# Performance work log

Measured on AMD Instinct MI355X. Metric: run time of the kernel, lower is better.

## Reference

```python
import jax, jax.numpy as jnp
import numpy as np

# --- fan-beam (flat detector) FBP geometry constants, matching init geo dict ---
V, U = 720, 736            # sino_views, nDetecU
NX = NY = 512              # nVoxelX, nVoxelY
SVOX = 400.0               # sVoxelX = sVoxelY (mm)
DU = 1.2858                # dDetecU (mm)
DSO, DOD = 595.0, 490.6    # source-origin, origin-detector distances
DSD = DSO + DOD
DBETA = 2.0 * np.pi / V    # angular step (full 2*pi scan, endpoint=False)


def _ramp_filter_fft():
    """Ram-Lak ramp filter (Kak & Slaney discrete spatial kernel), FFT'd for fast conv."""
    n = np.arange(-(U - 1), U)
    h = np.zeros(2 * U - 1, np.float64)
    h[U - 1] = 1.0 / (4.0 * DU * DU)
    odd = (np.abs(n) % 2 == 1)
    h[odd] = -1.0 / (np.pi * n[odd] * DU) ** 2
    L = int(2 ** np.ceil(np.log2(2 * (2 * U - 1))))  # zero-pad length (linear conv)
    return jnp.asarray(np.fft.fft(h, L).astype(np.complex64)), L

_HF, _L = _ramp_filter_fft()


def setup_inputs() -> dict:
    key = jax.random.key(0)
    sinogram = jax.random.uniform(key, (1, 1, V, U), dtype=jnp.float32)
    return {"sinogram": sinogram}


def reference(sinogram):
    # --- 1) cosine weighting of each detector sample ---
    sino = sinogram.reshape(V, U)
    us = (jnp.arange(U, dtype=jnp.float32) - (U - 1) / 2.0) * DU  # detector coords
    sino_w = sino * (DSD / jnp.sqrt(DSD * DSD + us * us))

    # --- 2) Ram-Lak ramp filtering per view (FFT linear convolution) ---
    Qf = jnp.fft.ifft(jnp.fft.fft(sino_w, n=_L, axis=1) * _HF[None, :], axis=1)
    Q = (jnp.real(Qf)[:, U - 1:2 * U - 1] * DU).astype(jnp.float32)  # [V, U]

    # --- 3) weighted fan-beam backprojection (scan over angles, O(Nx*Ny) carry) ---
    dx = SVOX / NX
    xs = (jnp.arange(NX, dtype=jnp.float32) - (NX - 1) / 2.0) * dx
    X, Y = jnp.meshgrid(xs, xs, indexing='ij')  # [NX, NY]
    betas = jnp.linspace(0.0, 2.0 * np.pi, V, endpoint=False).astype(jnp.float32)

    def body(img, ang_q):
        beta, q = ang_q                       # q: filtered projection [U]
        cb, sb = jnp.cos(beta), jnp.sin(beta)
        t = X * cb + Y * sb                   # coord along detector direction
        s = -X * sb + Y * cb                  # coord toward source
        D = DSO - s                           # source-to-pixel axial distance
        u = DSD * t / D                       # flat-detector intersection (mm)
        idx = u / DU + (U - 1) / 2.0          # fractional detector index
        i0 = jnp.clip(jnp.floor(idx), 0, U - 2).astype(jnp.int32)
        f = idx - i0
        val = q[i0] * (1.0 - f) + q[i0 + 1] * f
        val = jnp.where((idx >= 0.0) & (idx <= U - 1.0), val, 0.0)
        return img + (DSO / D) ** 2 * val, None

    img0 = jnp.zeros((NX, NY), jnp.float32)
    img, _ = jax.lax.scan(body, img0, (betas, Q))
    # 0.5 factor: full 2*pi fan scan covers each ray twice
    return (img * (0.5 * DBETA)).reshape(1, 1, NX, NY)
```

## Files before the change

kernel.cpp:

```cpp
#include <hip/hip_runtime.h>
#include <math.h>

#define NV 720
#define NU 736
#define NUP 768
#define NXY 512

__global__ __launch_bounds__(192) void filter_kernel(const float* __restrict__ sino,
                                                     float* __restrict__ Q,
                                                     float4* __restrict__ trig,
                                                     float* __restrict__ out_zero) {
    __shared__ float s4[2][368][4];
    __shared__ float wco[736];
    const int half = blockIdx.x & 1;
    const int vb = blockIdx.x >> 1;
    const int v0 = vb * 4;
    const int t = threadIdx.x;

    for (int i = blockIdx.x * 192 + t; i < NXY * NXY; i += 360 * 192)
        out_zero[i] = 0.0f;

    if (half == 0 && t < 4) {
        int v = v0 + t;
        float beta = (float)((double)v * (2.0 * M_PI / 720.0));
        float cb = cosf(beta), sb = sinf(beta);
        const float K = (float)(1085.6 / 1.2858);
        trig[v] = make_float4(cb * K, sb * K, cb, sb);
    }
    for (int i = t; i < 736; i += 192) {
        double n = (double)(2 * i - 735);
        double a = M_PI * n * 1.2858;
        wco[i] = (float)(-1.0 / (a * a));
    }
    const float DSD2 = (float)(1085.6 * 1085.6);
    for (int vv = 0; vv < 4; ++vv) {
        for (int u = t; u < 736; u += 192) {
            float us = ((float)u - 367.5f) * 1.2858f;
            float cw = 1085.6f / sqrtf(DSD2 + us * us);
            s4[u & 1][u >> 1][vv] = sino[(v0 + vv) * NU + u] * cw;
        }
    }
    __syncthreads();

    if (t < 184) {
        const int pj = (t < 92) ? 1 : 0;
        const int J0 = (t < 92) ? t : t - 92;
        const int q = 1 - pj;
        const int rb = half * 2;
        float acc[2][4];
        #pragma unroll
        for (int r = 0; r < 2; ++r)
            #pragma unroll
            for (int vv = 0; vv < 4; ++vv) acc[r][vv] = 0.0f;

        const int ibase0 = J0 + 367 + pj;
        #pragma unroll 4
        for (int m = 0; m < 368; ++m) {
            const float4 sv = *(const float4*)&s4[q][m][0];
            const int ib = ibase0 - m;
            const float w0 = wco[ib + 92 * rb];
            const float w1 = wco[ib + 92 * rb + 92];
            acc[0][0] = fmaf(w0, sv.x, acc[0][0]);
            acc[0][1] = fmaf(w0, sv.y, acc[0][1]);
            acc[0][2] = fmaf(w0, sv.z, acc[0][2]);
            acc[0][3] = fmaf(w0, sv.w, acc[0][3]);
            acc[1][0] = fmaf(w1, sv.x, acc[1][0]);
            acc[1][1] = fmaf(w1, sv.y, acc[1][1]);
            acc[1][2] = fmaf(w1, sv.z, acc[1][2]);
            acc[1][3] = fmaf(w1, sv.w, acc[1][3]);
        }
        const float H0 = (float)(1.0 / (4.0 * 1.2858 * 1.2858));
        #pragma unroll
        for (int r = 0; r < 2; ++r) {
            const float4 c = *(const float4*)&s4[pj][J0 + 92 * (rb + r)][0];
            acc[r][0] = fmaf(H0, c.x, acc[r][0]);
            acc[r][1] = fmaf(H0, c.y, acc[r][1]);
            acc[r][2] = fmaf(H0, c.z, acc[r][2]);
            acc[r][3] = fmaf(H0, c.w, acc[r][3]);
        }
        #pragma unroll
        for (int r = 0; r < 2; ++r) {
            const int j = 2 * (J0 + 92 * (rb + r)) + pj;
            #pragma unroll
            for (int vv = 0; vv < 4; ++vv)
                Q[(v0 + vv) * NUP + j] = acc[r][vv] * 1.2858f;
        }
    }
}

__global__ __launch_bounds__(256) void bp_kernel(const float* __restrict__ Q,
                                                 const float4* __restrict__ trig,
                                                 float* __restrict__ out) {
    __shared__ float win[2][4][NUP];
    const int b = blockIdx.x;
    const int c = b & 15;
    const int blk = b >> 4;
    const int bx = blk >> 4;
    const int by = blk & 15;
    const int t = threadIdx.x;
    const int w = t >> 6;
    const int l = t & 63;
    const int iq = (bx << 4) + ((w >> 1) << 3) + (l >> 3);
    const int jq = (by << 4) + ((w & 1) << 3) + (l & 7);

    const float dx = 400.0f / 512.0f;
    const float X = ((float)iq - 255.5f) * dx;
    const float Y = ((float)jq - 255.5f) * dx;
    const float Kc = (float)(1085.6 / 1.2858);

    float acc0 = 0.0f, acc1 = 0.0f, acc2 = 0.0f, acc3 = 0.0f;
    const bool inr = fmaf(X, X, Y * Y) <= 236.5f * 236.5f;
    const bool myint = __all(inr);

    const int nk = (c < 4) ? 12 : 11;
    const float* rowp = Q + (size_t)(c + 180 * w) * NUP;
    const float4* tvp = trig + c;

    #pragma unroll
    for (int ch = 0; ch < 3; ++ch)
        __builtin_amdgcn_global_load_lds(
            (const __attribute__((address_space(1))) void*)(rowp + ch * 256 + l * 4),
            (__attribute__((address_space(3))) void*)&win[0][w][ch * 256],
            16, 0, 0);

    for (int it = 0; it < nk; ++it) {
        __syncthreads();
        if (it + 1 < nk) {
            const float* rn = rowp + 16 * NUP;
            #pragma unroll
            for (int ch = 0; ch < 3; ++ch)
                __builtin_amdgcn_global_load_lds(
                    (const __attribute__((address_space(1))) void*)(rn + ch * 256 + l * 4),
                    (__attribute__((address_space(3))) void*)&win[(it + 1) & 1][w][ch * 256],
                    16, 0, 0);
        }
        const float* winf = &win[it & 1][0][0];

        if (myint) {
            const float4 tv = tvp[0];
            float a = fmaf(tv.z, X, tv.w * Y);
            float bb = fmaf(tv.z, Y, -tv.w * X);
            float aK = a * Kc, bK = bb * Kc;
            float D0 = 595.0f - bb, D1 = 595.0f + a, D2 = 595.0f + bb, D3 = 595.0f - a;
            float r0 = __builtin_amdgcn_rcpf(D0);
            float r1 = __builtin_amdgcn_rcpf(D1);
            float r2 = __builtin_amdgcn_rcpf(D2);
            float r3 = __builtin_amdgcn_rcpf(D3);
            float fi0 = fmaf(aK,  r0, 367.5f);
            float fi1 = fmaf(bK,  r1, 367.5f);
            float fi2 = fmaf(-aK, r2, 367.5f);
            float fi3 = fmaf(-bK, r3, 367.5f);
            int im[4] = {(int)fi0, (int)fi1, (int)fi2, (int)fi3};
            float ff[4] = {__builtin_amdgcn_fractf(fi0), __builtin_amdgcn_fractf(fi1),
                           __builtin_amdgcn_fractf(fi2), __builtin_amdgcn_fractf(fi3)};
            float gg[4] = {r0 * r0, r1 * r1, r2 * r2, r3 * r3};
            float* accp[4] = {&acc0, &acc1, &acc2, &acc3};
            #pragma unroll
            for (int m = 0; m < 4; ++m) {
                #pragma unroll
                for (int k = 0; k < 4; ++k) {
                    const float* p = winf + (k * NUP + im[m]);
                    float q0 = p[0];
                    float q1 = p[1];
                    float val = fmaf(ff[m], q1 - q0, q0);
                    *accp[(m - k) & 3] = fmaf(gg[m], val, *accp[(m - k) & 3]);
                }
            }
        } else {
            const float4 tvs[4] = {tvp[0], tvp[180], tvp[360], tvp[540]};
            const float pX[4] = {X, Y, -X, -Y};
            const float pY[4] = {Y, -X, -Y, X};
            float* accp[4] = {&acc0, &acc1, &acc2, &acc3};
            #pragma unroll
            for (int j = 0; j < 4; ++j) {
                float Xm = pX[j], Ym = pY[j];
                #pragma unroll
                for (int k = 0; k < 4; ++k) {
                    const float4 tv = tvs[k];
                    float t2 = fmaf(tv.x, Xm, tv.y * Ym);
                    float D  = fmaf(tv.w, Xm, fmaf(tv.z, -Ym, 595.0f));
                    float rD = __builtin_amdgcn_rcpf(D);
                    float fidx = fmaf(t2, rD, 367.5f);
                    int i0c = min(max((int)fidx, 0), NU - 2);
                    float f = __builtin_amdgcn_fractf(fidx);
                    const float* p = winf + (k * NUP + i0c);
                    float q0 = p[0];
                    float q1 = p[1];
                    float val = fmaf(f, q1 - q0, q0);
                    float cen = fidx - 367.5f;
                    float g = (__builtin_fabsf(cen) <= 367.5f) ? rD * rD : 0.0f;
                    *accp[j] = fmaf(g, val, *accp[j]);
                }
            }
        }
        rowp += 16 * NUP;
        tvp += 16;
    }
    const float SC = (float)(595.0 * 595.0 * 0.5 * (2.0 * M_PI / 720.0));
    const int ir = 511 - iq, jr = 511 - jq;
    unsafeAtomicAdd(&out[iq * NXY + jq], acc0 * SC);
    unsafeAtomicAdd(&out[jq * NXY + ir], acc1 * SC);
    unsafeAtomicAdd(&out[ir * NXY + jr], acc2 * SC);
    unsafeAtomicAdd(&out[jr * NXY + iq], acc3 * SC);
}

extern "C" void kernel_launch(void* const* d_in, const int* in_sizes, int n_in,
                              void* d_out, int out_size, void* d_ws, size_t ws_size,
                              hipStream_t stream) {
    const float* sino = (const float*)d_in[0];
    float* out = (float*)d_out;
    float* Q = (float*)d_ws;
    float4* trig = (float4*)((char*)d_ws + (size_t)NV * NUP * sizeof(float));

    filter_kernel<<<360, 192, 0, stream>>>(sino, Q, trig, out);
    bp_kernel<<<4096, 256, 0, stream>>>(Q, trig, out);
}
```

Before: 116.1 us.

## Split filter convolution across four thread groups with readlane broadcast and LDS reduction

The ramp-filter kernel now launches 720 blocks of 512 threads instead of 360 blocks of 192. Each block handles one quarter of the output detector range for four views. The 368-tap sum is split across four 128-thread groups, each covering 92 taps. Sinogram samples are held in registers and broadcast with readlane instead of being re-read from LDS, and partial sums are combined through a shared-memory reduction. The aim is more parallelism and less LDS traffic in the filter stage, at the cost of an extra barrier, wasted lanes (only 92 of each 128 are active), and more launched blocks.

```diff
diff --git a/kernel.cpp b/kernel.cpp
--- a/kernel.cpp
+++ b/kernel.cpp
@@ -6,85 +6,129 @@
 #define NUP 768
 #define NXY 512
 
-__global__ __launch_bounds__(192) void filter_kernel(const float* __restrict__ sino,
-                                                     float* __restrict__ Q,
-                                                     float4* __restrict__ trig,
-                                                     float* __restrict__ out_zero) {
+__device__ __forceinline__ float rl(float v, int l) {
+    return __int_as_float(__builtin_amdgcn_readlane(__float_as_int(v), l));
+}
+#define KEEP(x) asm volatile("" : "+v"(x))
+
+__global__ __launch_bounds__(512, 6) void filter_kernel(const float* __restrict__ sino,
+                                                        float* __restrict__ Q,
+                                                        float4* __restrict__ trig,
+                                                        float* __restrict__ out_zero) {
     __shared__ float s4[2][368][4];
     __shared__ float wco[736];
-    const int half = blockIdx.x & 1;
-    const int vb = blockIdx.x >> 1;
+    __shared__ float part[3][128][8];
+    const int bx = blockIdx.x;
+    const int q = bx & 3;
+    const int vb = bx >> 2;
     const int v0 = vb * 4;
-    const int t = threadIdx.x;
-
-    for (int i = blockIdx.x * 192 + t; i < NXY * NXY; i += 360 * 192)
+    const int tid = threadIdx.x;
+    const int tz = tid >> 7;
+    const int tg = tid & 127;
+    const int lane = tid & 63;
+
+    for (int i = bx * 512 + tid; i < NXY * NXY; i += 720 * 512)
         out_zero[i] = 0.0f;
 
-    if (half == 0 && t < 4) {
-        int v = v0 + t;
+    if (q == 0 && tid < 4) {
+        int v = v0 + tid;
         float beta = (float)((double)v * (2.0 * M_PI / 720.0));
         float cb = cosf(beta), sb = sinf(beta);
         const float K = (float)(1085.6 / 1.2858);
         trig[v] = make_float4(cb * K, sb * K, cb, sb);
     }
-    for (int i = t; i < 736; i += 192) {
+    for (int i = tid; i < 736; i += 512) {
         double n = (double)(2 * i - 735);
         double a = M_PI * n * 1.2858;
         wco[i] = (float)(-1.0 / (a * a));
     }
     const float DSD2 = (float)(1085.6 * 1085.6);
-    for (int vv = 0; vv < 4; ++vv) {
-        for (int u = t; u < 736; u += 192) {
-            float us = ((float)u - 367.5f) * 1.2858f;
-            float cw = 1085.6f / sqrtf(DSD2 + us * us);
-            s4[u & 1][u >> 1][vv] = sino[(v0 + vv) * NU + u] * cw;
-        }
+    for (int u = tg; u < 736; u += 128) {
+        float us = ((float)u - 367.5f) * 1.2858f;
+        float cw = 1085.6f / sqrtf(DSD2 + us * us);
+        s4[u & 1][u >> 1][tz] = sino[(v0 + tz) * NU + u] * cw;
     }
     __syncthreads();
 
-    if (t < 184) {
-        const int pj = (t < 92) ? 1 : 0;
-        const int J0 = (t < 92) ? t : t - 92;
-        const int q = 1 - pj;
-        const int rb = half * 2;
-        float acc[2][4];
+    const int m0 = 92 * tz;
+    const int iA = m0 + lane;
+    const int iB = min(m0 + 64 + lane, 367);
+    float4 svA0 = *(const float4*)&s4[0][iA][0];
+    float4 svA1 = *(const float4*)&s4[1][iA][0];
+    float4 svB0 = *(const float4*)&s4[0][iB][0];
+    float4 svB1 = *(const float4*)&s4[1][iB][0];
+    KEEP(svA0.x); KEEP(svA0.y); KEEP(svA0.z); KEEP(svA0.w);
+    KEEP(svA1.x); KEEP(svA1.y); KEEP(svA1.z); KEEP(svA1.w);
+    KEEP(svB0.x); KEEP(svB0.y); KEEP(svB0.z); KEEP(svB0.w);
+    KEEP(svB1.x); KEEP(svB1.y); KEEP(svB1.z); KEEP(svB1.w);
+
+    float a00 = 0.f, a01 = 0.f, a02 = 0.f, a03 = 0.f;
+    float a10 = 0.f, a11 = 0.f, a12 = 0.f, a13 = 0.f;
+    const int J0 = tg;
+    const int J0c = min(J0, 91);
+
+    {
+        const int K0 = J0c + 92 * q + 367;
+        const float* wpA = &wco[K0 - m0];
+        #pragma unroll 4
+        for (int mm = 0; mm < 64; ++mm) {
+            const float* p = wpA - mm;
+            const float w0 = p[0];
+            const float w1 = p[1];
+            const float s1x = rl(svA1.x, mm), s1y = rl(svA1.y, mm),
+                        s1z = rl(svA1.z, mm), s1w = rl(svA1.w, mm);
+            const float s0x = rl(svA0.x, mm), s0y = rl(svA0.y, mm),
+                        s0z = rl(svA0.z, mm), s0w = rl(svA0.w, mm);
+            a00 = fmaf(w0, s1x, a00); a01 = fmaf(w0, s1y, a01);
+            a02 = fmaf(w0, s1z, a02); a03 = fmaf(w0, s1w, a03);
+            a10 = fmaf(w1, s0x, a10); a11 = fmaf(w1, s0y, a11);
+            a12 = fmaf(w1, s0z, a12); a13 = fmaf(w1, s0w, a13);
+        }
+        const float* wpB = wpA - 64;
+        #pragma unroll 4
+        for (int mm = 0; mm < 28; ++mm) {
+            const float* p = wpB - mm;
+            const float w0 = p[0];
+            const float w1 = p[1];
+            const float s1x = rl(svB1.x, mm), s1y = rl(svB1.y, mm),
+                        s1z = rl(svB1.z, mm), s1w = rl(svB1.w, mm);
+            const float s0x = rl(svB0.x, mm), s0y = rl(svB0.y, mm),
+                        s0z = rl(svB0.z, mm), s0w = rl(svB0.w, mm);
+            a00 = fmaf(w0, s1x, a00); a01 = fmaf(w0, s1y, a01);
+            a02 = fmaf(w0, s1z, a02); a03 = fmaf(w0, s1w, a03);
+            a10 = fmaf(w1, s0x, a10); a11 = fmaf(w1, s0y, a11);
+            a12 = fmaf(w1, s0z, a12); a13 = fmaf(w1, s0w, a13);
+        }
+    }
+
+    if (tz != 0 && J0 < 92) {
+        *(float4*)&part[tz - 1][J0][0] = make_float4(a00, a01, a02, a03);
+        *(float4*)&part[tz - 1][J0][4] = make_float4(a10, a11, a12, a13);
+    }
+    __syncthreads();
+
+    if (tz == 0 && J0 < 92) {
         #pragma unroll
-        for (int r = 0; r < 2; ++r)
-            #pragma unroll
-            for (int vv = 0; vv < 4; ++vv) acc[r][vv] = 0.0f;
-
-        const int ibase0 = J0 + 367 + pj;
-        #pragma unroll 4
-        for (int m = 0; m < 368; ++m) {
-            const float4 sv = *(const float4*)&s4[q][m][0];
-            const int ib = ibase0 - m;
-            const float w0 = wco[ib + 92 * rb];
-            const float w1 = wco[ib + 92 * rb + 92];
-            acc[0][0] = fmaf(w0, sv.x, acc[0][0]);
-            acc[0][1] = fmaf(w0, sv.y, acc[0][1]);
-            acc[0][2] = fmaf(w0, sv.z, acc[0][2]);
-            acc[0][3] = fmaf(w0, sv.w, acc[0][3]);
-            acc[1][0] = fmaf(w1, sv.x, acc[1][0]);
-            acc[1][1] = fmaf(w1, sv.y, acc[1][1]);
-            acc[1][2] = fmaf(w1, sv.z, acc[1][2]);
-            acc[1][3] = fmaf(w1, sv.w, acc[1][3]);
+        for (int g = 0; g < 3; ++g) {
+            const float4 p0 = *(const float4*)&part[g][J0][0];
+            const float4 p1 = *(const float4*)&part[g][J0][4];
+            a00 += p0.x; a01 += p0.y; a02 += p0.z; a03 += p0.w;
+            a10 += p1.x; a11 += p1.y; a12 += p1.z; a13 += p1.w;
         }
         const float H0 = (float)(1.0 / (4.0 * 1.2858 * 1.2858));
-        #pragma unroll
-        for (int r = 0; r < 2; ++r) {
-            const float4 c = *(const float4*)&s4[pj][J0 + 92 * (rb + r)][0];
-            acc[r][0] = fmaf(H0, c.x, acc[r][0]);
-            acc[r][1] = fmaf(H0, c.y, acc[r][1]);
-            acc[r][2] = fmaf(H0, c.z, acc[r][2]);
-            acc[r][3] = fmaf(H0, c.w, acc[r][3]);
-        }
-        #pragma unroll
-        for (int r = 0; r < 2; ++r) {
-            const int j = 2 * (J0 + 92 * (rb + r)) + pj;
-            #pragma unroll
-            for (int vv = 0; vv < 4; ++vv)
-                Q[(v0 + vv) * NUP + j] = acc[r][vv] * 1.2858f;
-        }
+        const int jh = J0 + 92 * q;
+        const float4 c0 = *(const float4*)&s4[0][jh][0];
+        const float4 c1 = *(const float4*)&s4[1][jh][0];
+        a00 = fmaf(H0, c0.x, a00); a01 = fmaf(H0, c0.y, a01);
+        a02 = fmaf(H0, c0.z, a02); a03 = fmaf(H0, c0.w, a03);
+        a10 = fmaf(H0, c1.x, a10); a11 = fmaf(H0, c1.y, a11);
+        a12 = fmaf(H0, c1.z, a12); a13 = fmaf(H0, c1.w, a13);
+        const int j0i = 2 * jh;
+        const float DU = 1.2858f;
+        Q[(v0 + 0) * NUP + j0i] = a00 * DU;  Q[(v0 + 0) * NUP + j0i + 1] = a10 * DU;
+        Q[(v0 + 1) * NUP + j0i] = a01 * DU;  Q[(v0 + 1) * NUP + j0i + 1] = a11 * DU;
+        Q[(v0 + 2) * NUP + j0i] = a02 * DU;  Q[(v0 + 2) * NUP + j0i + 1] = a12 * DU;
+        Q[(v0 + 3) * NUP + j0i] = a03 * DU;  Q[(v0 + 3) * NUP + j0i + 1] = a13 * DU;
     }
 }
 
@@ -212,6 +256,6 @@
     float* Q = (float*)d_ws;
     float4* trig = (float4*)((char*)d_ws + (size_t)NV * NUP * sizeof(float));
 
-    filter_kernel<<<360, 192, 0, stream>>>(sino, Q, trig, out);
+    filter_kernel<<<720, 512, 0, stream>>>(sino, Q, trig, out);
     bp_kernel<<<4096, 256, 0, stream>>>(Q, trig, out);
 }
```

Result: slower. 122.7 us (+5.7%).

## Split filter into prep and split-K convolution kernel with shared-memory reduction

Applied to the files above, without the earlier changes.

Moves cosine weighting, trig table and output zeroing into a separate prep kernel that writes an interleaved weighted sinogram to workspace. The filter kernel then runs on 720 blocks of 512 threads. The 368-tap convolution is split four ways across thread groups, and the partial sums are reduced in shared memory, which shortens the serial dependency chain and raises parallelism. In exchange it adds a kernel launch, a global round-trip for the weighted data, and redundant clamped work for threads with J0 of 92 or more.

```diff
diff --git a/kernel.cpp b/kernel.cpp
--- a/kernel.cpp
+++ b/kernel.cpp
@@ -5,86 +5,105 @@
 #define NU 736
 #define NUP 768
 #define NXY 512
-
-__global__ __launch_bounds__(192) void filter_kernel(const float* __restrict__ sino,
-                                                     float* __restrict__ Q,
-                                                     float4* __restrict__ trig,
-                                                     float* __restrict__ out_zero) {
-    __shared__ float s4[2][368][4];
-    __shared__ float wco[736];
-    const int half = blockIdx.x & 1;
-    const int vb = blockIdx.x >> 1;
-    const int v0 = vb * 4;
-    const int t = threadIdx.x;
-
-    for (int i = blockIdx.x * 192 + t; i < NXY * NXY; i += 360 * 192)
-        out_zero[i] = 0.0f;
-
-    if (half == 0 && t < 4) {
-        int v = v0 + t;
+#define NM 368
+
+__global__ __launch_bounds__(368) void prep_kernel(const float* __restrict__ sino,
+                                                   float* __restrict__ swI,
+                                                   float4* __restrict__ trig,
+                                                   float* __restrict__ out_zero) {
+    const int v = blockIdx.x;
+    const int m = threadIdx.x;
+    const int vb = v >> 2, vv = v & 3;
+    const float DSD2 = (float)(1085.6 * 1085.6);
+    #pragma unroll
+    for (int pu = 0; pu < 2; ++pu) {
+        const int u = 2 * m + pu;
+        float us = ((float)u - 367.5f) * 1.2858f;
+        float cw = 1085.6f / sqrtf(DSD2 + us * us);
+        swI[((size_t)vb * NM + m) * 8 + pu * 4 + vv] = sino[v * NU + u] * cw;
+    }
+    if (m == 0) {
         float beta = (float)((double)v * (2.0 * M_PI / 720.0));
         float cb = cosf(beta), sb = sinf(beta);
         const float K = (float)(1085.6 / 1.2858);
         trig[v] = make_float4(cb * K, sb * K, cb, sb);
     }
-    for (int i = t; i < 736; i += 192) {
+    for (int i = v * 368 + m; i < NXY * NXY; i += 720 * 368)
+        out_zero[i] = 0.0f;
+}
+
+__global__ __launch_bounds__(512) void filter_kernel(const float* __restrict__ swI,
+                                                     float* __restrict__ Q) {
+    __shared__ float wco[736];
+    __shared__ float part[3][8][96];
+    const int bx = blockIdx.x;
+    const int q = bx & 3;
+    const int vb = bx >> 2;
+    const int v0 = vb * 4;
+    const int tid = threadIdx.x;
+    const int J0 = tid & 127;
+
+    for (int i = tid; i < 736; i += 512) {
         double n = (double)(2 * i - 735);
         double a = M_PI * n * 1.2858;
         wco[i] = (float)(-1.0 / (a * a));
     }
-    const float DSD2 = (float)(1085.6 * 1085.6);
-    for (int vv = 0; vv < 4; ++vv) {
-        for (int u = t; u < 736; u += 192) {
-            float us = ((float)u - 367.5f) * 1.2858f;
-            float cw = 1085.6f / sqrtf(DSD2 + us * us);
-            s4[u & 1][u >> 1][vv] = sino[(v0 + vv) * NU + u] * cw;
-        }
-    }
     __syncthreads();
 
-    if (t < 184) {
-        const int pj = (t < 92) ? 1 : 0;
-        const int J0 = (t < 92) ? t : t - 92;
-        const int q = 1 - pj;
-        const int rb = half * 2;
-        float acc[2][4];
+    const int m0 = __builtin_amdgcn_readfirstlane(92 * (tid >> 7));
+    const int tz = m0 / 92;
+    const float* sw = swI + (size_t)vb * NM * 8;
+    const float* sp = sw + (size_t)m0 * 8;
+
+    float a00 = 0.f, a01 = 0.f, a02 = 0.f, a03 = 0.f;
+    float a10 = 0.f, a11 = 0.f, a12 = 0.f, a13 = 0.f;
+    const int J0c = min(J0, 91);
+    const int y0 = J0c + 367 + 92 * q;
+    const float* wp = &wco[y0 - m0];
+
+    #pragma unroll 4
+    for (int mm = 0; mm < 92; ++mm) {
+        const float w0 = wp[-mm];
+        const float w1 = wp[1 - mm];
+        const float* s = sp + mm * 8;
+        const float s10 = s[4], s11 = s[5], s12 = s[6], s13 = s[7];
+        const float s00 = s[0], s01 = s[1], s02 = s[2], s03 = s[3];
+        a00 = fmaf(w0, s10, a00); a01 = fmaf(w0, s11, a01);
+        a02 = fmaf(w0, s12, a02); a03 = fmaf(w0, s13, a03);
+        a10 = fmaf(w1, s00, a10); a11 = fmaf(w1, s01, a11);
+        a12 = fmaf(w1, s02, a12); a13 = fmaf(w1, s03, a13);
+    }
+
+    if (tz != 0 && J0 < 92) {
+        part[tz - 1][0][J0] = a00; part[tz - 1][1][J0] = a01;
+        part[tz - 1][2][J0] = a02; part[tz - 1][3][J0] = a03;
+        part[tz - 1][4][J0] = a10; part[tz - 1][5][J0] = a11;
+        part[tz - 1][6][J0] = a12; part[tz - 1][7][J0] = a13;
+    }
+    __syncthreads();
+
+    if (tz == 0 && J0 < 92) {
         #pragma unroll
-        for (int r = 0; r < 2; ++r)
-            #pragma unroll
-            for (int vv = 0; vv < 4; ++vv) acc[r][vv] = 0.0f;
-
-        const int ibase0 = J0 + 367 + pj;
-        #pragma unroll 4
-        for (int m = 0; m < 368; ++m) {
-            const float4 sv = *(const float4*)&s4[q][m][0];
-            const int ib = ibase0 - m;
-            const float w0 = wco[ib + 92 * rb];
-            const float w1 = wco[ib + 92 * rb + 92];
-            acc[0][0] = fmaf(w0, sv.x, acc[0][0]);
-            acc[0][1] = fmaf(w0, sv.y, acc[0][1]);
-            acc[0][2] = fmaf(w0, sv.z, acc[0][2]);
-            acc[0][3] = fmaf(w0, sv.w, acc[0][3]);
-            acc[1][0] = fmaf(w1, sv.x, acc[1][0]);
-            acc[1][1] = fmaf(w1, sv.y, acc[1][1]);
-            acc[1][2] = fmaf(w1, sv.z, acc[1][2]);
-            acc[1][3] = fmaf(w1, sv.w, acc[1][3]);
+        for (int g = 0; g < 3; ++g) {
+            a00 += part[g][0][J0]; a01 += part[g][1][J0];
+            a02 += part[g][2][J0]; a03 += part[g][3][J0];
+            a10 += part[g][4][J0]; a11 += part[g][5][J0];
+            a12 += part[g][6][J0]; a13 += part[g][7][J0];
         }
         const float H0 = (float)(1.0 / (4.0 * 1.2858 * 1.2858));
-        #pragma unroll
-        for (int r = 0; r < 2; ++r) {
-            const float4 c = *(const float4*)&s4[pj][J0 + 92 * (rb + r)][0];
-            acc[r][0] = fmaf(H0, c.x, acc[r][0]);
-            acc[r][1] = fmaf(H0, c.y, acc[r][1]);
-            acc[r][2] = fmaf(H0, c.z, acc[r][2]);
-            acc[r][3] = fmaf(H0, c.w, acc[r][3]);
-        }
-        #pragma unroll
-        for (int r = 0; r < 2; ++r) {
-            const int j = 2 * (J0 + 92 * (rb + r)) + pj;
-            #pragma unroll
-            for (int vv = 0; vv < 4; ++vv)
-                Q[(v0 + vv) * NUP + j] = acc[r][vv] * 1.2858f;
-        }
+        const int mc = J0 + 92 * q;
+        const float4 c0 = *(const float4*)(sw + (size_t)mc * 8);
+        const float4 c1 = *(const float4*)(sw + (size_t)mc * 8 + 4);
+        a00 = fmaf(H0, c0.x, a00); a01 = fmaf(H0, c0.y, a01);
+        a02 = fmaf(H0, c0.z, a02); a03 = fmaf(H0, c0.w, a03);
+        a10 = fmaf(H0, c1.x, a10); a11 = fmaf(H0, c1.y, a11);
+        a12 = fmaf(H0, c1.z, a12); a13 = fmaf(H0, c1.w, a13);
+        const int j0i = 2 * (J0 + 92 * q);
+        const float DU = 1.2858f;
+        *(float2*)&Q[(v0 + 0) * NUP + j0i] = make_float2(a00 * DU, a10 * DU);
+        *(float2*)&Q[(v0 + 1) * NUP + j0i] = make_float2(a01 * DU, a11 * DU);
+        *(float2*)&Q[(v0 + 2) * NUP + j0i] = make_float2(a02 * DU, a12 * DU);
+        *(float2*)&Q[(v0 + 3) * NUP + j0i] = make_float2(a03 * DU, a13 * DU);
     }
 }
 
@@ -211,7 +230,9 @@
     float* out = (float*)d_out;
     float* Q = (float*)d_ws;
     float4* trig = (float4*)((char*)d_ws + (size_t)NV * NUP * sizeof(float));
-
-    filter_kernel<<<360, 192, 0, stream>>>(sino, Q, trig, out);
+    float* swI = (float*)((char*)trig + (size_t)NV * sizeof(float4));
+
+    prep_kernel<<<720, 368, 0, stream>>>(sino, swI, trig, out);
+    filter_kernel<<<720, 512, 0, stream>>>(swI, Q);
     bp_kernel<<<4096, 256, 0, stream>>>(Q, trig, out);
 }
```

After: 117.5 us. No clear change (+1.2%).
